# Kernel optimization log

Measured on AMD Instinct MI355X. Metric: run time of the kernel, lower is better.

The kernel has to match this reference:

```python
import jax, jax.numpy as jnp
import numpy as np

EPS = 1e-6          # torch F.pairwise_distance default eps (added to the difference)
NORM_EPS = 1e-12    # torch F.normalize default eps
CORRECT_W = 1.0
INCORRECT_W = 0.0001


def _l2norm(x):
    return x / jnp.maximum(jnp.linalg.norm(x, axis=1, keepdims=True), NORM_EPS)


def setup_inputs() -> dict:
    key = jax.random.key(0)
    k1, k2, k3 = jax.random.split(key, 3)
    N, D, R = 1048576, 128, 53
    model_output = jax.random.normal(k1, (N, D), dtype=jnp.float32)
    target = _l2norm(jax.random.normal(k2, (N, D), dtype=jnp.float32))
    # RelationEmbedding stores row-normalized embeddings
    relation_embeds = _l2norm(jax.random.normal(k3, (R, D), dtype=jnp.float32))
    return {"model_output": model_output, "target": target, "relation_embeds": relation_embeds}


def reference(model_output, target, relation_embeds):
    # F.normalize(model_output, p=2, dim=1)
    mo = _l2norm(model_output)

    # correct term: sum_i || mo_i - target_i + eps ||_2
    correct = jnp.sum(jnp.sqrt(jnp.sum((mo - target + EPS) ** 2, axis=1)))

    # incorrect term: for each row, max over relations of || mo_i - emb_r + eps ||_2.
    # Expand || d + eps ||^2 = ||d||^2 + 2*eps*sum(d) + D*eps^2 to avoid an [N,R,D] tensor.
    D = mo.shape[1]
    mo_sq = jnp.sum(mo * mo, axis=1)                       # [N]
    re_sq = jnp.sum(relation_embeds * relation_embeds, axis=1)  # [R]
    dots = mo @ relation_embeds.T                          # [N, R]
    mo_sum = jnp.sum(mo, axis=1)                           # [N]
    re_sum = jnp.sum(relation_embeds, axis=1)              # [R]
    sq = (mo_sq[:, None] + re_sq[None, :] - 2.0 * dots
          + 2.0 * EPS * (mo_sum[:, None] - re_sum[None, :])
          + D * EPS * EPS)                                 # [N, R]
    dist = jnp.sqrt(jnp.maximum(sq, 0.0))
    incorrect = jnp.sum(jnp.max(dist, axis=1))

    return CORRECT_W * correct + INCORRECT_W * (1.0 - incorrect)
```

## Files before the change

kernel.cpp:

```cpp
#include <hip/hip_runtime.h>

typedef __attribute__((ext_vector_type(8))) short short8;
typedef __attribute__((ext_vector_type(4))) float f32x4;

#define EPS 1e-6f
#define NB 2048

static __device__ __forceinline__ short f2bf(float f) {
    unsigned u = __float_as_uint(f);
    unsigned r = (u + 0x7FFFu + ((u >> 16) & 1u)) >> 16;
    return (short)(unsigned short)r;
}

__global__ void prep_kernel(const float* __restrict__ re, short* __restrict__ re_bf,
                            float* __restrict__ re_c2, int R) {
    int tid = threadIdx.x;
    int r = tid >> 2, q = tid & 3;
    float v[32];
    if (r < R) {
        const float* p = re + (size_t)r * 128 + q * 32;
#pragma unroll
        for (int j = 0; j < 32; ++j) v[j] = p[j];
    } else {
#pragma unroll
        for (int j = 0; j < 32; ++j) v[j] = 0.f;
    }
    float ssq = 0.f, sum = 0.f;
#pragma unroll
    for (int j = 0; j < 32; ++j) { ssq = fmaf(v[j], v[j], ssq); sum += v[j]; }
    ssq += __shfl_xor(ssq, 1); ssq += __shfl_xor(ssq, 2);
    sum += __shfl_xor(sum, 1); sum += __shfl_xor(sum, 2);
    short* o = re_bf + r * 128 + q * 32;
#pragma unroll
    for (int j = 0; j < 32; ++j) o[j] = f2bf(v[j]);
    if (q == 0) re_c2[r] = (r < R) ? (ssq - 2.f * EPS * sum) : -1e30f;
}

__global__ __launch_bounds__(256) void loss_main(
    const float* __restrict__ mo, const float* __restrict__ tg,
    const short* __restrict__ re_bf, const float* __restrict__ re_c2,
    float* __restrict__ partials, int nrows) {
    const int tid = threadIdx.x;
    const int lane = tid & 63;
    const int widx = tid >> 6;
    const int col16 = lane & 15;
    const int kg = lane >> 4;
    const int ko = kg * 8;

    __shared__ short8 bf_lds[16][64];
    if (widx == 0) {
#pragma unroll
        for (int rt = 0; rt < 4; ++rt)
#pragma unroll
            for (int s = 0; s < 4; ++s)
                bf_lds[rt * 4 + s][lane] = *reinterpret_cast<const short8*>(
                    re_bf + (rt * 16 + col16) * 128 + s * 32 + ko);
    }
    float rc[4][4];
#pragma unroll
    for (int rt = 0; rt < 4; ++rt)
#pragma unroll
        for (int reg = 0; reg < 4; ++reg)
            rc[rt][reg] = re_c2[rt * 16 + kg * 4 + reg];
    __syncthreads();

    float corr_acc = 0.f, inc_acc = 0.f;
    const int NT = nrows >> 4;
    const int nw = gridDim.x * 4;
    int t = blockIdx.x * 4 + widx;

    if (t < NT) {
        alignas(16) float x[32];

        {
            const float* rp = mo + ((size_t)(t * 16 + col16) * 128 + ko);
#pragma unroll
            for (int s = 0; s < 4; ++s) {
                *(f32x4*)(x + s * 8)     = *(const f32x4*)(rp + s * 32);
                *(f32x4*)(x + s * 8 + 4) = *(const f32x4*)(rp + s * 32 + 4);
            }
        }

        while (t < NT) {
            alignas(16) float tv[32];
            {
                const float* tp = tg + ((size_t)(t * 16 + col16) * 128 + ko);
#pragma unroll
                for (int s = 0; s < 4; ++s) {
                    *(f32x4*)(tv + s * 8)     = *(const f32x4*)(tp + s * 32);
                    *(f32x4*)(tv + s * 8 + 4) = *(const f32x4*)(tp + s * 32 + 4);
                }
            }

            float ssq = 0.f, sum = 0.f;
#pragma unroll
            for (int j = 0; j < 32; ++j) { ssq = fmaf(x[j], x[j], ssq); sum += x[j]; }
            float xt = 0.f, tsq = 0.f, tsum = 0.f;
#pragma unroll
            for (int j = 0; j < 32; ++j) {
                xt  = fmaf(x[j], tv[j], xt);
                tsq = fmaf(tv[j], tv[j], tsq);
                tsum += tv[j];
            }
            ssq  += __shfl_xor(ssq, 16);  ssq  += __shfl_xor(ssq, 32);
            sum  += __shfl_xor(sum, 16);  sum  += __shfl_xor(sum, 32);
            xt   += __shfl_xor(xt, 16);   xt   += __shfl_xor(xt, 32);
            tsq  += __shfl_xor(tsq, 16);  tsq  += __shfl_xor(tsq, 32);
            tsum += __shfl_xor(tsum, 16); tsum += __shfl_xor(tsum, 32);

            float rnorm  = 1.0f / fmaxf(sqrtf(ssq), 1e-12f);
            float mo_sq  = ssq * rnorm * rnorm;
            float mo_sum = sum * rnorm;
            float mconst = fmaf(2.f * EPS, mo_sum, mo_sq) + 128.f * EPS * EPS;

            float cs = mconst + tsq - 2.f * EPS * tsum - 2.f * rnorm * xt;
            if (kg == 0) corr_acc += sqrtf(fmaxf(cs, 0.f));

            short8 afrag[4];
#pragma unroll
            for (int s = 0; s < 4; ++s)
#pragma unroll
                for (int j = 0; j < 8; ++j)
                    afrag[s][j] = f2bf(x[s * 8 + j] * rnorm);

            int t2 = t + nw;
            if (t2 < NT) {
                const float* rp = mo + ((size_t)(t2 * 16 + col16) * 128 + ko);
#pragma unroll
                for (int s = 0; s < 4; ++s) {
                    *(f32x4*)(x + s * 8)     = *(const f32x4*)(rp + s * 32);
                    *(f32x4*)(x + s * 8 + 4) = *(const f32x4*)(rp + s * 32 + 4);
                }
            }

            float vmax = -1e30f;
#pragma unroll
            for (int rt = 0; rt < 4; ++rt) {
                f32x4 acc = {0.f, 0.f, 0.f, 0.f};
#pragma unroll
                for (int s = 0; s < 4; ++s)
                    acc = __builtin_amdgcn_mfma_f32_16x16x32_bf16(
                        bf_lds[rt * 4 + s][lane], afrag[s], acc, 0, 0, 0);
#pragma unroll
                for (int reg = 0; reg < 4; ++reg) {
                    float d2 = mconst + rc[rt][reg] - 2.f * acc[reg];
                    vmax = fmaxf(vmax, d2);
                }
            }
            vmax = fmaxf(vmax, __shfl_xor(vmax, 16));
            vmax = fmaxf(vmax, __shfl_xor(vmax, 32));
            if (kg == 0) inc_acc += sqrtf(fmaxf(vmax, 0.f));

            t = t2;
        }
    }

    __shared__ float redc[256];
    __shared__ float redi[256];
    redc[tid] = corr_acc; redi[tid] = inc_acc;
    __syncthreads();
    for (int s = 128; s > 0; s >>= 1) {
        if (tid < s) { redc[tid] += redc[tid + s]; redi[tid] += redi[tid + s]; }
        __syncthreads();
    }
    if (tid == 0) {
        partials[blockIdx.x * 2]     = redc[0];
        partials[blockIdx.x * 2 + 1] = redi[0];
    }
}

__global__ void final_kernel(const float* __restrict__ partials, float* __restrict__ out, int nb) {
    __shared__ float rc_[256];
    __shared__ float ri_[256];
    int tid = threadIdx.x;
    float c = 0.f, ic = 0.f;
    for (int i = tid; i < nb; i += 256) { c += partials[2 * i]; ic += partials[2 * i + 1]; }
    rc_[tid] = c; ri_[tid] = ic;
    __syncthreads();
    for (int s = 128; s > 0; s >>= 1) {
        if (tid < s) { rc_[tid] += rc_[tid + s]; ri_[tid] += ri_[tid + s]; }
        __syncthreads();
    }
    if (tid == 0) out[0] = rc_[0] + 1e-4f * (1.f - ri_[0]);
}

extern "C" void kernel_launch(void* const* d_in, const int* in_sizes, int n_in,
                              void* d_out, int out_size, void* d_ws, size_t ws_size,
                              hipStream_t stream) {
    const float* mo = (const float*)d_in[0];
    const float* tg = (const float*)d_in[1];
    const float* re = (const float*)d_in[2];
    const int D = 128;
    const int nrows = in_sizes[0] / D;
    const int R = in_sizes[2] / D;

    char* ws = (char*)d_ws;
    short* re_bf    = (short*)ws;
    float* re_c2    = (float*)(ws + 16384);
    float* partials = (float*)(ws + 16896);

    prep_kernel<<<1, 256, 0, stream>>>(re, re_bf, re_c2, R);
    loss_main<<<NB, 256, 0, stream>>>(mo, tg, re_bf, re_c2, partials, nrows);
    final_kernel<<<1, 256, 0, stream>>>(partials, (float*)d_out, NB);
}
```

Before: 188.2 us.

## Double-buffer row tiles via direct global-to-LDS loads with one-wave blocks

Switches to 64-thread single-wave blocks, raises the grid to 8192, and streams each 16-row tile of model_output and target into a swizzled double-buffered LDS region using global_load_lds. The next-next tile is prefetched while the current one is computed. Relation fragments move from shared memory into registers, and the final block reduction becomes a wave shuffle. The aim is to hide HBM latency on this bandwidth-bound loop, at the cost of 32 KB LDS per one-wave block, which may limit occupancy, plus hand-written waitcnt counts that must match the number of issued loads.

Measured after the change: 217.1 us. 1.15x slower.

```diff
diff --git a/kernel.cpp b/kernel.cpp
--- a/kernel.cpp
+++ b/kernel.cpp
@@ -1,10 +1,11 @@
 #include <hip/hip_runtime.h>
+#include <hip/hip_bf16.h>
 
 typedef __attribute__((ext_vector_type(8))) short short8;
 typedef __attribute__((ext_vector_type(4))) float f32x4;
 
 #define EPS 1e-6f
-#define NB 2048
+#define NBLK 8192
 
 static __device__ __forceinline__ short f2bf(float f) {
     unsigned u = __float_as_uint(f);
@@ -36,61 +37,84 @@
     if (q == 0) re_c2[r] = (r < R) ? (ssq - 2.f * EPS * sum) : -1e30f;
 }
 
-__global__ __launch_bounds__(256) void loss_main(
+__global__ __launch_bounds__(64) void loss_main(
     const float* __restrict__ mo, const float* __restrict__ tg,
     const short* __restrict__ re_bf, const float* __restrict__ re_c2,
     float* __restrict__ partials, int nrows) {
-    const int tid = threadIdx.x;
-    const int lane = tid & 63;
-    const int widx = tid >> 6;
+    __shared__ char lds[32768] __attribute__((aligned(16)));
+    const int lane = threadIdx.x;
     const int col16 = lane & 15;
     const int kg = lane >> 4;
     const int ko = kg * 8;
 
-    __shared__ short8 bf_lds[16][64];
-    if (widx == 0) {
-#pragma unroll
-        for (int rt = 0; rt < 4; ++rt)
-#pragma unroll
-            for (int s = 0; s < 4; ++s)
-                bf_lds[rt * 4 + s][lane] = *reinterpret_cast<const short8*>(
-                    re_bf + (rt * 16 + col16) * 128 + s * 32 + ko);
-    }
+    short8 bfrag[4][4];
     float rc[4][4];
 #pragma unroll
-    for (int rt = 0; rt < 4; ++rt)
+    for (int rt = 0; rt < 4; ++rt) {
+#pragma unroll
+        for (int s = 0; s < 4; ++s)
+            bfrag[rt][s] = *reinterpret_cast<const short8*>(
+                re_bf + (rt * 16 + col16) * 128 + s * 32 + ko);
 #pragma unroll
         for (int reg = 0; reg < 4; ++reg)
             rc[rt][reg] = re_c2[rt * 16 + kg * 4 + reg];
-    __syncthreads();
-
+    }
+
+    const int NT = nrows >> 4;
+    const int stride = gridDim.x;
+    const int t0 = blockIdx.x;
     float corr_acc = 0.f, inc_acc = 0.f;
-    const int NT = nrows >> 4;
-    const int nw = gridDim.x * 4;
-    int t = blockIdx.x * 4 + widx;
-
-    if (t < NT) {
-        alignas(16) float x[32];
-
-        {
-            const float* rp = mo + ((size_t)(t * 16 + col16) * 128 + ko);
+
+    const int roff = col16 * 512 + kg * 32;
+    const int swz  = (col16 & 7) << 4;
+
+    auto stage = [&](int t, int p) {
+        const char* mo_b = (const char*)mo + (size_t)t * 8192;
+        const char* tg_b = (const char*)tg + (size_t)t * 8192;
+        char* lbase = (char*)lds + p * 16384;
+#pragma unroll
+        for (int j = 0; j < 8; ++j) {
+            int lin = j * 1024 + lane * 16;
+            int g = lin ^ (((lin >> 9) & 7) << 4);
+            __builtin_amdgcn_global_load_lds(
+                (const __attribute__((address_space(1))) void*)(mo_b + g),
+                (__attribute__((address_space(3))) void*)(lbase + j * 1024), 16, 0, 0);
+            __builtin_amdgcn_global_load_lds(
+                (const __attribute__((address_space(1))) void*)(tg_b + g),
+                (__attribute__((address_space(3))) void*)(lbase + 8192 + j * 1024), 16, 0, 0);
+        }
+    };
+
+    if (t0 < NT) {
+        asm volatile("s_waitcnt vmcnt(0)" ::: "memory");
+        __builtin_amdgcn_sched_barrier(0);
+        stage(t0, 0);
+        if (t0 + stride < NT) stage(t0 + stride, 1);
+        int p = 0;
+
+        for (int t = t0; t < NT; t += stride) {
+            const bool nxt   = (t + stride) < NT;
+            const bool more2 = (t + 2 * stride) < NT;
+            if (nxt) { asm volatile("s_waitcnt vmcnt(16)" ::: "memory"); }
+            else     { asm volatile("s_waitcnt vmcnt(0)"  ::: "memory"); }
+            __builtin_amdgcn_sched_barrier(0);
+
+            const char* lb = (const char*)lds + p * 16384;
+            alignas(16) float x[32];
+            alignas(16) float tv[32];
 #pragma unroll
             for (int s = 0; s < 4; ++s) {
-                *(f32x4*)(x + s * 8)     = *(const f32x4*)(rp + s * 32);
-                *(f32x4*)(x + s * 8 + 4) = *(const f32x4*)(rp + s * 32 + 4);
-            }
-        }
-
-        while (t < NT) {
-            alignas(16) float tv[32];
-            {
-                const float* tp = tg + ((size_t)(t * 16 + col16) * 128 + ko);
-#pragma unroll
-                for (int s = 0; s < 4; ++s) {
-                    *(f32x4*)(tv + s * 8)     = *(const f32x4*)(tp + s * 32);
-                    *(f32x4*)(tv + s * 8 + 4) = *(const f32x4*)(tp + s * 32 + 4);
-                }
-            }
+                *(f32x4*)(x + s * 8)      = *(const f32x4*)(lb + ((roff + s * 128)      ^ swz));
+                *(f32x4*)(x + s * 8 + 4)  = *(const f32x4*)(lb + ((roff + s * 128 + 16) ^ swz));
+            }
+#pragma unroll
+            for (int s = 0; s < 4; ++s) {
+                *(f32x4*)(tv + s * 8)     = *(const f32x4*)(lb + 8192 + ((roff + s * 128)      ^ swz));
+                *(f32x4*)(tv + s * 8 + 4) = *(const f32x4*)(lb + 8192 + ((roff + s * 128 + 16) ^ swz));
+            }
+            asm volatile("s_waitcnt lgkmcnt(0)" ::: "memory");
+            __builtin_amdgcn_sched_barrier(0);
+            if (more2) stage(t + 2 * stride, p);
 
             float ssq = 0.f, sum = 0.f;
 #pragma unroll
@@ -121,17 +145,7 @@
             for (int s = 0; s < 4; ++s)
 #pragma unroll
                 for (int j = 0; j < 8; ++j)
-                    afrag[s][j] = f2bf(x[s * 8 + j] * rnorm);
-
-            int t2 = t + nw;
-            if (t2 < NT) {
-                const float* rp = mo + ((size_t)(t2 * 16 + col16) * 128 + ko);
-#pragma unroll
-                for (int s = 0; s < 4; ++s) {
-                    *(f32x4*)(x + s * 8)     = *(const f32x4*)(rp + s * 32);
-                    *(f32x4*)(x + s * 8 + 4) = *(const f32x4*)(rp + s * 32 + 4);
-                }
-            }
+                    afrag[s][j] = __builtin_bit_cast(short, __float2bfloat16(x[s * 8 + j] * rnorm));
 
             float vmax = -1e30f;
 #pragma unroll
@@ -140,7 +154,7 @@
 #pragma unroll
                 for (int s = 0; s < 4; ++s)
                     acc = __builtin_amdgcn_mfma_f32_16x16x32_bf16(
-                        bf_lds[rt * 4 + s][lane], afrag[s], acc, 0, 0, 0);
+                        bfrag[rt][s], afrag[s], acc, 0, 0, 0);
 #pragma unroll
                 for (int reg = 0; reg < 4; ++reg) {
                     float d2 = mconst + rc[rt][reg] - 2.f * acc[reg];
@@ -151,21 +165,18 @@
             vmax = fmaxf(vmax, __shfl_xor(vmax, 32));
             if (kg == 0) inc_acc += sqrtf(fmaxf(vmax, 0.f));
 
-            t = t2;
+            p ^= 1;
         }
     }
 
-    __shared__ float redc[256];
-    __shared__ float redi[256];
-    redc[tid] = corr_acc; redi[tid] = inc_acc;
-    __syncthreads();
-    for (int s = 128; s > 0; s >>= 1) {
-        if (tid < s) { redc[tid] += redc[tid + s]; redi[tid] += redi[tid + s]; }
-        __syncthreads();
-    }
-    if (tid == 0) {
-        partials[blockIdx.x * 2]     = redc[0];
-        partials[blockIdx.x * 2 + 1] = redi[0];
+#pragma unroll
+    for (int m = 1; m < 16; m <<= 1) {
+        corr_acc += __shfl_xor(corr_acc, m);
+        inc_acc  += __shfl_xor(inc_acc, m);
+    }
+    if (lane == 0) {
+        partials[blockIdx.x * 2]     = corr_acc;
+        partials[blockIdx.x * 2 + 1] = inc_acc;
     }
 }
 
@@ -200,6 +211,6 @@
     float* partials = (float*)(ws + 16896);
 
     prep_kernel<<<1, 256, 0, stream>>>(re, re_bf, re_c2, R);
-    loss_main<<<NB, 256, 0, stream>>>(mo, tg, re_bf, re_c2, partials, nrows);
-    final_kernel<<<1, 256, 0, stream>>>(partials, (float*)d_out, NB);
-}
+    loss_main<<<NBLK, 64, 0, stream>>>(mo, tg, re_bf, re_c2, partials, nrows);
+    final_kernel<<<1, 256, 0, stream>>>(partials, (float*)d_out, NBLK);
+}
```
